# Optimization experiments

Measured on AMD Instinct MI355X. Metric: run time of the kernel, lower is better.

Reference implementation:

```python
import jax, jax.numpy as jnp
import numpy as np

EPS = 1e-6
D_MODEL, D_HEAD, COND_F = 1024, 64, 768
N_HEADS = D_MODEL // D_HEAD
BATCH, SEQ = 2, 2048


def _rope_freqs(d_head, n_heads):
    # RoPE.__init__: dim = d_head // 2; count = n_heads * dim // 4 = n_heads * d_head // 8
    d8 = d_head // 8
    log_min, log_max = np.log(np.pi), np.log(10.0 * np.pi)
    f = np.exp(np.linspace(log_min, log_max, n_heads * d8 + 1, dtype=np.float64)[:-1])
    return jnp.asarray(f.reshape(d8, n_heads).T, dtype=jnp.float32)  # [nh, d8]


def _apply_rotary(x, theta):
    # x: [n, nh, l, e], theta: [n, nh, l, d8]; rotate first 2*d8 channels
    d = theta.shape[-1]
    x1, x2, rest = x[..., :d], x[..., d:2 * d], x[..., 2 * d:]
    cos, sin = jnp.cos(theta), jnp.sin(theta)
    y1 = x1 * cos - x2 * sin
    y2 = x2 * cos + x1 * sin
    return jnp.concatenate([y1, y2, rest], axis=-1)


def setup_inputs() -> dict:
    key = jax.random.key(0)
    ks = jax.random.split(key, 6)
    x = jax.random.normal(ks[0], (BATCH, SEQ, D_MODEL), dtype=jnp.float32)
    pos = jnp.broadcast_to(jnp.arange(SEQ, dtype=jnp.float32), (BATCH, SEQ))[..., None]
    cond = jax.random.normal(ks[1], (BATCH, COND_F), dtype=jnp.float32)
    w_norm = jax.random.normal(ks[2], (D_MODEL, COND_F), dtype=jnp.float32) * 0.02
    w_qkv = jax.random.normal(ks[3], (3 * D_MODEL, D_MODEL), dtype=jnp.float32) * 0.02
    scale = jnp.full((N_HEADS,), 10.0, dtype=jnp.float32)
    w_out = jax.random.normal(ks[4], (D_MODEL, D_MODEL), dtype=jnp.float32) * 0.02
    return {"x": x, "pos": pos, "cond": cond, "w_norm": w_norm,
            "w_qkv": w_qkv, "scale": scale, "w_out": w_out}


def reference(x, pos, cond, w_norm, w_qkv, scale, w_out):
    n, l, d = x.shape
    nh, e = N_HEADS, D_HEAD
    skip = x
    # AdaRMSNorm: scale = (linear(cond) + 1) * rsqrt(mean(x^2))
    cond_scale = cond @ w_norm.T + 1.0                      # [n, d]
    mean_sq = jnp.mean(x * x, axis=-1, keepdims=True)       # [n, l, 1]
    xn = x * (cond_scale[:, None, :] * jax.lax.rsqrt(mean_sq + EPS))
    # QKV projection
    qkv = (xn @ w_qkv.T).reshape(n, l, 3, nh, e)
    q = jnp.transpose(qkv[:, :, 0], (0, 2, 1, 3))           # [n, nh, l, e]
    k = jnp.transpose(qkv[:, :, 1], (0, 2, 1, 3))
    v = jnp.transpose(qkv[:, :, 2], (0, 2, 1, 3))
    # cosine-sim scaling
    sqrt_scale = jnp.sqrt(scale)[None, :, None, None]       # [1, nh, 1, 1]
    q = q * (sqrt_scale * jax.lax.rsqrt(jnp.sum(q * q, axis=-1, keepdims=True) + EPS))
    k = k * (sqrt_scale * jax.lax.rsqrt(jnp.sum(k * k, axis=-1, keepdims=True) + EPS))
    # RoPE: theta = pos[..., None] * freqs -> [n, l, nh, d8] -> [n, nh, l, d8]
    freqs = _rope_freqs(e, nh)
    theta = jnp.transpose(pos[..., None] * freqs, (0, 2, 1, 3))
    q = _apply_rotary(q, theta)
    k = _apply_rotary(k, theta)
    # attention with softmax scale = 1.0
    scores = jnp.einsum('nhle,nhme->nhlm', q, k)
    attn = jax.nn.softmax(scores, axis=-1)
    out = jnp.einsum('nhlm,nhme->nhle', attn, v)
    out = jnp.transpose(out, (0, 2, 1, 3)).reshape(n, l, d)
    return out @ w_out.T + skip
```

## Files before the change

### kernel.cpp

```cpp
#include <hip/hip_runtime.h>
#include <math.h>

#define D_MODEL 1024
#define D_HEAD  64
#define N_HEADS 16
#define COND_F  768
#define BATCH   2
#define SEQ     2048
#define NTOK    (BATCH*SEQ)
#define QKV_N   (3*D_MODEL)

typedef unsigned short u16;
typedef __attribute__((ext_vector_type(4))) float  f32x4;
typedef __attribute__((ext_vector_type(8))) __bf16 bfrag;
typedef __attribute__((ext_vector_type(4))) unsigned short u16x4;
typedef __attribute__((ext_vector_type(8))) unsigned short u16x8;

__device__ __forceinline__ u16 f2bf(float f) {
    unsigned u = __builtin_bit_cast(unsigned, f);
    return (u16)((u + 0x7fffu + ((u >> 16) & 1u)) >> 16);
}
__device__ __forceinline__ float bf2f(u16 h) {
    unsigned u = ((unsigned)h) << 16;
    return __builtin_bit_cast(float, u);
}

__device__ __forceinline__ float fexp2(float x) {
    float y;
    asm("v_exp_f32 %0, %1" : "=v"(y) : "v"(x));
    return y;
}

__device__ __forceinline__ void async16(const void* g, void* l) {
    __builtin_amdgcn_global_load_lds(
        (const __attribute__((address_space(1))) unsigned int*)g,
        (__attribute__((address_space(3))) unsigned int*)l, 16, 0, 0);
}

__global__ __launch_bounds__(256) void prep_kernel(const float* __restrict__ wqkv,
                                                   const float* __restrict__ wout,
                                                   u16* __restrict__ wqkv_b,
                                                   u16* __restrict__ wout_b,
                                                   const float* __restrict__ cond,
                                                   const float* __restrict__ w_norm,
                                                   float* __restrict__ cs,
                                                   const float* __restrict__ pos,
                                                   float2* __restrict__ tab) {
    if (blockIdx.x < 2048) {
        int i = blockIdx.x * 256 + threadIdx.x;
        const int n1 = QKV_N * D_MODEL / 8;
        const float* src; u16* dst; int off;
        if (i < n1) { src = wqkv; dst = wqkv_b; off = i * 8; }
        else        { src = wout; dst = wout_b; off = (i - n1) * 8; }
        float4 a = *(const float4*)(src + off);
        float4 b = *(const float4*)(src + off + 4);
        *(u16x4*)(dst + off)     = (u16x4){f2bf(a.x), f2bf(a.y), f2bf(a.z), f2bf(a.w)};
        *(u16x4*)(dst + off + 4) = (u16x4){f2bf(b.x), f2bf(b.y), f2bf(b.z), f2bf(b.w)};
    } else if (blockIdx.x < 2560) {
        int lane = threadIdx.x & 63, w = threadIdx.x >> 6;
        int wid = (blockIdx.x - 2048) * 4 + w;
        int b = wid >> 10, d = wid & 1023;
        const float* c = cond + b * COND_F;
        const float* wn = w_norm + (size_t)d * COND_F;
        float acc = 0.f;
        #pragma unroll
        for (int kk = 0; kk < 3; ++kk) {
            int j = kk * 256 + lane * 4;
            float4 cv = *(const float4*)(c + j);
            float4 wv = *(const float4*)(wn + j);
            acc += cv.x * wv.x + cv.y * wv.y + cv.z * wv.z + cv.w * wv.w;
        }
        for (int m = 1; m < 64; m <<= 1) acc += __shfl_xor(acc, m);
        if (lane == 0) cs[wid] = acc + 1.0f;
    } else {
        int i = (blockIdx.x - 2560) * 256 + threadIdx.x;
        int j = i & 7, h = (i >> 3) & 15;
        int s = (i >> 7) & 2047, b = i >> 18;
        double lf = 1.1447298858494001741 + (double)(j * 16 + h) * (2.302585092994045684 / 128.0);
        float fr = (float)exp(lf);
        float th = pos[b * SEQ + s] * fr;
        tab[i] = make_float2(cosf(th), sinf(th));
    }
}

__global__ __launch_bounds__(256) void rmsnorm_kernel(const float* __restrict__ x,
                                                      const float* __restrict__ cs,
                                                      u16* __restrict__ xn) {
    int tok = blockIdx.x, t = threadIdx.x;
    int b = tok >> 11;
    const float* xr = x + (size_t)tok * D_MODEL;
    float4 v = *(const float4*)(xr + t * 4);
    float ss = v.x * v.x + v.y * v.y + v.z * v.z + v.w * v.w;
    for (int m = 1; m < 64; m <<= 1) ss += __shfl_xor(ss, m);
    __shared__ float red[4];
    int w = t >> 6;
    if ((t & 63) == 0) red[w] = ss;
    __syncthreads();
    float tot = red[0] + red[1] + red[2] + red[3];
    float r = rsqrtf(tot * (1.0f / D_MODEL) + 1e-6f);
    float4 cv = *(const float4*)(cs + b * D_MODEL + t * 4);
    *(u16x4*)(xn + (size_t)tok * D_MODEL + t * 4) =
        (u16x4){f2bf(v.x * cv.x * r), f2bf(v.y * cv.y * r),
                f2bf(v.z * cv.z * r), f2bf(v.w * cv.w * r)};
}

template<int NT, int MODE>
__global__ __launch_bounds__(256) void gemm_bt(const u16* __restrict__ A, const u16* __restrict__ B,
                                               u16* __restrict__ Cq, u16* __restrict__ Ck,
                                               u16* __restrict__ Cv, float* __restrict__ Cf,
                                               const float* __restrict__ skip,
                                               const float* __restrict__ scale,
                                               const float2* __restrict__ tab,
                                               int M, int N, int K) {
    __shared__ u16 As0[128 * 32];
    __shared__ u16 As1[128 * 32];
    __shared__ u16 Bs0[NT * 32];
    __shared__ u16 Bs1[NT * 32];
    constexpr int FN = NT / 32;
    int tid = threadIdx.x;
    int lane = tid & 63, w = tid >> 6;
    int wr = w >> 1;
    int wc = w & 1;
    int m0 = blockIdx.x * 128, n0 = blockIdx.y * NT;
    f32x4 acc[4][FN] = {};
    const u16* Ag = A + (size_t)m0 * K;
    const u16* Bg = B + (size_t)n0 * K;
    int lr = lane & 15, lq = lane >> 4;

    #define GSTAGE(kt, Ad, Bd) do { \
        _Pragma("unroll") \
        for (int i = 0; i < 2; ++i) { \
            int c = i * 256 + tid; int row = c >> 2, col = c & 3; \
            async16(Ag + (size_t)row * K + (kt) + col * 8, Ad + c * 8); \
        } \
        _Pragma("unroll") \
        for (int i = 0; i < NT / 64; ++i) { \
            int c = i * 256 + tid; int row = c >> 2, col = c & 3; \
            async16(Bg + (size_t)row * K + (kt) + col * 8, Bd + c * 8); \
        } } while (0)

    auto compute = [&](const u16* Asb, const u16* Bsb) {
        bfrag af[4], bfv[FN];
        #pragma unroll
        for (int fm = 0; fm < 4; ++fm)
            af[fm] = *(const bfrag*)&Asb[(wr * 64 + fm * 16 + lr) * 32 + lq * 8];
        #pragma unroll
        for (int fn = 0; fn < FN; ++fn)
            bfv[fn] = *(const bfrag*)&Bsb[(wc * (NT / 2) + fn * 16 + lr) * 32 + lq * 8];
        #pragma unroll
        for (int fm = 0; fm < 4; ++fm)
            #pragma unroll
            for (int fn = 0; fn < FN; ++fn)
                acc[fm][fn] = __builtin_amdgcn_mfma_f32_16x16x32_bf16(af[fm], bfv[fn], acc[fm][fn], 0, 0, 0);
    };

    const int NK = K / 32;
    GSTAGE(0, As0, Bs0);
    __syncthreads();

    for (int t = 0; t < NK; t += 2) {
        if (t + 1 < NK) GSTAGE((t + 1) * 32, As1, Bs1);
        compute(As0, Bs0);
        __syncthreads();
        if (t + 2 < NK) GSTAGE((t + 2) * 32, As0, Bs0);
        if (t + 1 < NK) {
            compute(As1, Bs1);
            __syncthreads();
        }
    }
    #undef GSTAGE

    if (MODE == 1) {
        #pragma unroll
        for (int fm = 0; fm < 4; ++fm)
            #pragma unroll
            for (int fn = 0; fn < FN; ++fn) {
                int rowbase = m0 + wr * 64 + fm * 16 + lq * 4;
                int colbase = n0 + wc * (NT / 2) + fn * 16;
                #pragma unroll
                for (int r = 0; r < 4; ++r) {
                    int row = rowbase + r, col = colbase + lr;
                    Cf[(size_t)row * N + col] = acc[fm][fn][r] + skip[(size_t)row * N + col];
                }
            }
    } else {
        int colbase0 = n0 + wc * 64;
        int sel = colbase0 >> 10;
        int h = (colbase0 >> 6) & 15;
        int bb = m0 >> 11;
        if (sel == 2) {
            #pragma unroll
            for (int fm = 0; fm < 4; ++fm) {
                int sP = (m0 & 2047) + wr * 64 + (fm >> 1) * 32 + 8 * lq + 4 * (fm & 1);
                #pragma unroll
                for (int fn = 0; fn < 4; ++fn) {
                    int e = fn * 16 + lr;
                    u16x4 pk = {f2bf(acc[fm][fn][0]), f2bf(acc[fm][fn][1]),
                                f2bf(acc[fm][fn][2]), f2bf(acc[fm][fn][3])};
                    *(u16x4*)&Cv[((size_t)(bb * N_HEADS + h) * D_HEAD + e) * SEQ + sP] = pk;
                }
            }
        } else {
            u16* p = sel ? Ck : Cq;
            float sq = sqrtf(scale[h]);
            float mult = (sel == 0) ? sq * 1.4426950408889634f : sq;
            #pragma unroll
            for (int fm = 0; fm < 4; ++fm) {
                int s0 = (m0 & 2047) + wr * 64 + fm * 16 + lq * 4;
                #pragma unroll
                for (int r = 0; r < 4; ++r) {
                    float v0 = acc[fm][0][r], v1 = acc[fm][1][r],
                          v2 = acc[fm][2][r], v3 = acc[fm][3][r];
                    float ss = v0 * v0 + v1 * v1 + v2 * v2 + v3 * v3;
                    ss += __shfl_xor(ss, 1); ss += __shfl_xor(ss, 2);
                    ss += __shfl_xor(ss, 4); ss += __shfl_xor(ss, 8);
                    float rs = mult * rsqrtf(ss + 1e-6f);
                    v0 *= rs; v1 *= rs; v2 *= rs; v3 *= rs;
                    float part = __shfl_xor(v0, 8);
                    float2 cs2 = tab[(((size_t)bb * SEQ + (s0 + r)) * 16 + h) * 8 + (lr & 7)];
                    v0 = (lr < 8) ? v0 * cs2.x - part * cs2.y
                                  : v0 * cs2.x + part * cs2.y;
                    size_t rp = ((size_t)(bb * N_HEADS + h) * SEQ + (s0 + r)) * D_HEAD;
                    p[rp + lr]      = f2bf(v0);
                    p[rp + 16 + lr] = f2bf(v1);
                    p[rp + 32 + lr] = f2bf(v2);
                    p[rp + 48 + lr] = f2bf(v3);
                }
            }
        }
    }
}

__global__ __launch_bounds__(512) void attn_kernel(const u16* __restrict__ q,
                                                   const u16* __restrict__ k,
                                                   const u16* __restrict__ vt,
                                                   u16* __restrict__ o_part,
                                                   float* __restrict__ lsum_part) {
    __shared__ u16 Ks0[64 * 64];
    __shared__ u16 Ks1[64 * 64];
    __shared__ u16 Vs0[64 * 64];
    __shared__ u16 Vs1[64 * 64];
    int tid = threadIdx.x, lane = tid & 63, w = tid >> 6;
    int bh = blockIdx.y;
    int qs = blockIdx.x * 256;
    int z = blockIdx.z, nz = gridDim.z;
    int chunk = SEQ / nz;
    int kv0 = z * chunk;
    int lr = lane & 15, lq = lane >> 4;

    bfrag qf[2][2];
    #pragma unroll
    for (int mf = 0; mf < 2; ++mf) {
        const u16* qb = q + ((size_t)bh * SEQ + qs + w * 32 + mf * 16 + lr) * D_HEAD + lq * 8;
        qf[mf][0] = *(const bfrag*)qb;
        qf[mf][1] = *(const bfrag*)(qb + 32);
    }
    bfrag ones;
    #pragma unroll
    for (int j = 0; j < 8; ++j) ones[j] = (__bf16)1.0f;

    f32x4 oacc[2][4] = {};
    f32x4 oacc5[2] = {};
    const u16* kbase = k + (size_t)bh * SEQ * D_HEAD;
    const u16* vbase = vt + (size_t)bh * D_HEAD * SEQ;

    int srow = tid >> 3, scol = (tid & 7) ^ ((tid >> 3) & 7);
    const u16* kg = kbase + (size_t)srow * 64 + scol * 8;
    const u16* vg = vbase + (size_t)srow * SEQ + scol * 8;

    #define STAGE(kt, Kd, Vd) do { \
        async16(kg + (size_t)(kt) * 64, Kd + tid * 8); \
        async16(vg + (kt),              Vd + tid * 8); } while (0)

    auto tile_compute = [&](const u16* Kb, const u16* Vb) {
        f32x4 sacc[2][4] = {};
        __builtin_amdgcn_s_setprio(1);
        #pragma unroll
        for (int nb = 0; nb < 4; ++nb) {
            int row = nb * 16 + lr;
            #pragma unroll
            for (int kb = 0; kb < 2; ++kb) {
                bfrag kf = *(const bfrag*)&Kb[row * 64 + (((kb * 4 + lq) ^ (row & 7)) * 8)];
                sacc[0][nb] = __builtin_amdgcn_mfma_f32_16x16x32_bf16(kf, qf[0][kb], sacc[0][nb], 0, 0, 0);
                sacc[1][nb] = __builtin_amdgcn_mfma_f32_16x16x32_bf16(kf, qf[1][kb], sacc[1][nb], 0, 0, 0);
            }
        }
        __builtin_amdgcn_s_setprio(0);

        #pragma unroll
        for (int kb = 0; kb < 2; ++kb) {
            bfrag pf[2];
            #pragma unroll
            for (int mf = 0; mf < 2; ++mf)
                #pragma unroll
                for (int half = 0; half < 2; ++half) {
                    int nb = kb * 2 + half;
                    #pragma unroll
                    for (int r = 0; r < 4; ++r)
                        pf[mf][half * 4 + r] = (__bf16)fexp2(sacc[mf][nb][r]);
                }
            __builtin_amdgcn_s_setprio(1);
            oacc5[0] = __builtin_amdgcn_mfma_f32_16x16x32_bf16(pf[0], ones, oacc5[0], 0, 0, 0);
            oacc5[1] = __builtin_amdgcn_mfma_f32_16x16x32_bf16(pf[1], ones, oacc5[1], 0, 0, 0);
            #pragma unroll
            for (int eb = 0; eb < 4; ++eb) {
                int row = eb * 16 + lr;
                bfrag vf = *(const bfrag*)&Vb[row * 64 + (((kb * 4 + lq) ^ (row & 7)) * 8)];
                oacc[0][eb] = __builtin_amdgcn_mfma_f32_16x16x32_bf16(pf[kb == 0 ? 0 : 0], vf, oacc[0][eb], 0, 0, 0);
                oacc[1][eb] = __builtin_amdgcn_mfma_f32_16x16x32_bf16(pf[1], vf, oacc[1][eb], 0, 0, 0);
            }
            __builtin_amdgcn_s_setprio(0);
        }
    };

    STAGE(kv0, Ks0, Vs0);
    __syncthreads();

    const int NTILE = chunk / 64;
    for (int t = 0; t < NTILE; t += 2) {
        if (t + 1 < NTILE) STAGE(kv0 + (t + 1) * 64, Ks1, Vs1);
        tile_compute(Ks0, Vs0);
        __syncthreads();
        if (t + 2 < NTILE) STAGE(kv0 + (t + 2) * 64, Ks0, Vs0);
        if (t + 1 < NTILE) {
            tile_compute(Ks1, Vs1);
            __syncthreads();
        }
    }
    #undef STAGE

    int b = bh >> 4, h = bh & 15;
    u16* op = o_part + (size_t)z * NTOK * D_MODEL;
    #pragma unroll
    for (int mf = 0; mf < 2; ++mf) {
        #pragma unroll
        for (int r = 0; r < 4; ++r) {
            int qrow = qs + w * 32 + mf * 16 + lq * 4 + r;
            if (lr == 0)
                lsum_part[((size_t)z * BATCH * N_HEADS + bh) * SEQ + qrow] = oacc5[mf][r];
            #pragma unroll
            for (int eb = 0; eb < 4; ++eb) {
                int e = eb * 16 + lr;
                op[((size_t)b * SEQ + qrow) * D_MODEL + h * D_HEAD + e] = f2bf(oacc[mf][eb][r]);
            }
        }
    }
}

__global__ __launch_bounds__(256) void combine_kernel(const u16* __restrict__ o_part,
                                                      const float* __restrict__ lsum_part,
                                                      u16* __restrict__ out, int Z) {
    int i = blockIdx.x * 256 + threadIdx.x;
    int base = i * 8;
    int t = base >> 10, col = base & 1023;
    int b = t >> 11, s = t & 2047, h = col >> 6;
    size_t li = (size_t)(b * N_HEADS + h) * SEQ + s;
    float lsum = 0.f;
    for (int z = 0; z < Z; ++z) lsum += lsum_part[(size_t)z * BATCH * N_HEADS * SEQ + li];
    float inv = 1.0f / lsum;
    float acc[8] = {};
    for (int z = 0; z < Z; ++z) {
        u16x8 a = *(const u16x8*)(o_part + (size_t)z * NTOK * D_MODEL + base);
        #pragma unroll
        for (int j = 0; j < 8; ++j) acc[j] += bf2f(a[j]);
    }
    u16x8 r;
    #pragma unroll
    for (int j = 0; j < 8; ++j) r[j] = f2bf(acc[j] * inv);
    *(u16x8*)(out + base) = r;
}

extern "C" void kernel_launch(void* const* d_in, const int* in_sizes, int n_in,
                              void* d_out, int out_size, void* d_ws, size_t ws_size,
                              hipStream_t stream) {
    const float* x      = (const float*)d_in[0];
    const float* pos    = (const float*)d_in[1];
    const float* cond   = (const float*)d_in[2];
    const float* w_norm = (const float*)d_in[3];
    const float* w_qkv  = (const float*)d_in[4];
    const float* scale  = (const float*)d_in[5];
    const float* w_out  = (const float*)d_in[6];
    float* out = (float*)d_out;

    char* ws = (char*)d_ws;
    u16* xn     = (u16*)ws;
    u16* wqkv_b = (u16*)(ws + (8u  << 20));
    u16* wout_b = (u16*)(ws + (14u << 20));
    float* cs   = (float*)(ws + (16u << 20));
    u16* qb     = (u16*)(ws + (16u << 20) + (1u << 16));
    const size_t HSZ = (size_t)BATCH * N_HEADS * SEQ * D_HEAD;
    u16* kb = qb + HSZ;
    u16* vt = kb + HSZ;
    u16* o_part   = (u16*)(ws + (41u << 20));
    float2* tab   = (float2*)(ws + (41u << 20));
    u16* attn_o = xn;

    size_t need4 = (41ull << 20) + 4 * ((size_t)NTOK * D_MODEL * 2) + 4 * ((size_t)BATCH * N_HEADS * SEQ * 4);
    int Z = (ws_size >= need4) ? 4 : 2;
    float* lsum_p = (float*)(ws + (41u << 20) + (size_t)Z * NTOK * D_MODEL * 2);

    prep_kernel<<<dim3(4608), dim3(256), 0, stream>>>(w_qkv, w_out, wqkv_b, wout_b,
                                                      cond, w_norm, cs, pos, (float2*)tab);
    rmsnorm_kernel<<<dim3(NTOK), dim3(256), 0, stream>>>(x, cs, xn);
    gemm_bt<128, 0><<<dim3(NTOK / 128, QKV_N / 128), dim3(256), 0, stream>>>(
        xn, wqkv_b, qb, kb, vt, (float*)nullptr, (const float*)nullptr,
        scale, (const float2*)tab, NTOK, QKV_N, D_MODEL);
    attn_kernel<<<dim3(SEQ / 256, BATCH * N_HEADS, Z), dim3(512), 0, stream>>>(
        qb, kb, vt, o_part, lsum_p);
    combine_kernel<<<dim3(NTOK * D_MODEL / 8 / 256), dim3(256), 0, stream>>>(o_part, lsum_p, attn_o, Z);
    gemm_bt<64, 1><<<dim3(NTOK / 128, D_MODEL / 64), dim3(256), 0, stream>>>(
        attn_o, wout_b, nullptr, nullptr, nullptr, out, x,
        (const float*)nullptr, (const float2*)nullptr, NTOK, D_MODEL, D_MODEL);
}
```

Before: 128.9 us.

## Simplify GEMM to single-buffered 128x64 tiles with one row strip per wave

Replaces the double-buffered GEMM, which overlapped async loads with MFMA compute, with a single-buffered loop. That loop syncs twice per 32-wide K step and gives each wave a 32x64 output strip. The QKV projection now uses 128x64 tiles instead of 128x128, which doubles the grid and lowers per-block register and LDS use. This may help occupancy but gives up load/compute overlap and cuts operand reuse from shared memory. A no-op index expression in the attention kernel is also cleaned up.

```diff
diff --git a/kernel.cpp b/kernel.cpp
--- a/kernel.cpp
+++ b/kernel.cpp
@@ -104,7 +104,7 @@
                 f2bf(v.z * cv.z * r), f2bf(v.w * cv.w * r)};
 }
 
-template<int NT, int MODE>
+template<int MODE>
 __global__ __launch_bounds__(256) void gemm_bt(const u16* __restrict__ A, const u16* __restrict__ B,
                                                u16* __restrict__ Cq, u16* __restrict__ Ck,
                                                u16* __restrict__ Cv, float* __restrict__ Cf,
@@ -112,86 +112,59 @@
                                                const float* __restrict__ scale,
                                                const float2* __restrict__ tab,
                                                int M, int N, int K) {
-    __shared__ u16 As0[128 * 32];
-    __shared__ u16 As1[128 * 32];
-    __shared__ u16 Bs0[NT * 32];
-    __shared__ u16 Bs1[NT * 32];
-    constexpr int FN = NT / 32;
+    __shared__ u16 As[128 * 32];
+    __shared__ u16 Bs[64 * 32];
     int tid = threadIdx.x;
     int lane = tid & 63, w = tid >> 6;
-    int wr = w >> 1;
-    int wc = w & 1;
-    int m0 = blockIdx.x * 128, n0 = blockIdx.y * NT;
-    f32x4 acc[4][FN] = {};
+    int m0 = blockIdx.x * 128, n0 = blockIdx.y * 64;
+    f32x4 acc[2][4] = {};
     const u16* Ag = A + (size_t)m0 * K;
     const u16* Bg = B + (size_t)n0 * K;
     int lr = lane & 15, lq = lane >> 4;
 
-    #define GSTAGE(kt, Ad, Bd) do { \
-        _Pragma("unroll") \
-        for (int i = 0; i < 2; ++i) { \
-            int c = i * 256 + tid; int row = c >> 2, col = c & 3; \
-            async16(Ag + (size_t)row * K + (kt) + col * 8, Ad + c * 8); \
-        } \
-        _Pragma("unroll") \
-        for (int i = 0; i < NT / 64; ++i) { \
-            int c = i * 256 + tid; int row = c >> 2, col = c & 3; \
-            async16(Bg + (size_t)row * K + (kt) + col * 8, Bd + c * 8); \
-        } } while (0)
-
-    auto compute = [&](const u16* Asb, const u16* Bsb) {
-        bfrag af[4], bfv[FN];
-        #pragma unroll
-        for (int fm = 0; fm < 4; ++fm)
-            af[fm] = *(const bfrag*)&Asb[(wr * 64 + fm * 16 + lr) * 32 + lq * 8];
-        #pragma unroll
-        for (int fn = 0; fn < FN; ++fn)
-            bfv[fn] = *(const bfrag*)&Bsb[(wc * (NT / 2) + fn * 16 + lr) * 32 + lq * 8];
-        #pragma unroll
-        for (int fm = 0; fm < 4; ++fm)
-            #pragma unroll
-            for (int fn = 0; fn < FN; ++fn)
+    int c1 = 256 + tid;
+    for (int kt = 0; kt < K; kt += 32) {
+        __syncthreads();
+        async16(Ag + (size_t)(tid >> 2) * K + kt + (tid & 3) * 8, &As[tid * 8]);
+        async16(Ag + (size_t)(c1 >> 2) * K + kt + (c1 & 3) * 8, &As[c1 * 8]);
+        async16(Bg + (size_t)(tid >> 2) * K + kt + (tid & 3) * 8, &Bs[tid * 8]);
+        __syncthreads();
+        bfrag af[2], bfv[4];
+        #pragma unroll
+        for (int fm = 0; fm < 2; ++fm)
+            af[fm] = *(const bfrag*)&As[(w * 32 + fm * 16 + lr) * 32 + lq * 8];
+        #pragma unroll
+        for (int fn = 0; fn < 4; ++fn)
+            bfv[fn] = *(const bfrag*)&Bs[(fn * 16 + lr) * 32 + lq * 8];
+        #pragma unroll
+        for (int fm = 0; fm < 2; ++fm)
+            #pragma unroll
+            for (int fn = 0; fn < 4; ++fn)
                 acc[fm][fn] = __builtin_amdgcn_mfma_f32_16x16x32_bf16(af[fm], bfv[fn], acc[fm][fn], 0, 0, 0);
-    };
-
-    const int NK = K / 32;
-    GSTAGE(0, As0, Bs0);
-    __syncthreads();
-
-    for (int t = 0; t < NK; t += 2) {
-        if (t + 1 < NK) GSTAGE((t + 1) * 32, As1, Bs1);
-        compute(As0, Bs0);
-        __syncthreads();
-        if (t + 2 < NK) GSTAGE((t + 2) * 32, As0, Bs0);
-        if (t + 1 < NK) {
-            compute(As1, Bs1);
-            __syncthreads();
-        }
-    }
-    #undef GSTAGE
+    }
 
     if (MODE == 1) {
         #pragma unroll
-        for (int fm = 0; fm < 4; ++fm)
-            #pragma unroll
-            for (int fn = 0; fn < FN; ++fn) {
-                int rowbase = m0 + wr * 64 + fm * 16 + lq * 4;
-                int colbase = n0 + wc * (NT / 2) + fn * 16;
+        for (int fm = 0; fm < 2; ++fm) {
+            int rowbase = m0 + w * 32 + fm * 16 + lq * 4;
+            #pragma unroll
+            for (int fn = 0; fn < 4; ++fn) {
+                int col = n0 + fn * 16 + lr;
                 #pragma unroll
                 for (int r = 0; r < 4; ++r) {
-                    int row = rowbase + r, col = colbase + lr;
+                    int row = rowbase + r;
                     Cf[(size_t)row * N + col] = acc[fm][fn][r] + skip[(size_t)row * N + col];
                 }
             }
+        }
     } else {
-        int colbase0 = n0 + wc * 64;
-        int sel = colbase0 >> 10;
-        int h = (colbase0 >> 6) & 15;
+        int sel = n0 >> 10;
+        int h = (n0 >> 6) & 15;
         int bb = m0 >> 11;
         if (sel == 2) {
             #pragma unroll
-            for (int fm = 0; fm < 4; ++fm) {
-                int sP = (m0 & 2047) + wr * 64 + (fm >> 1) * 32 + 8 * lq + 4 * (fm & 1);
+            for (int fm = 0; fm < 2; ++fm) {
+                int sP = (m0 & 2047) + w * 32 + 8 * lq + 4 * fm;
                 #pragma unroll
                 for (int fn = 0; fn < 4; ++fn) {
                     int e = fn * 16 + lr;
@@ -205,8 +178,8 @@
             float sq = sqrtf(scale[h]);
             float mult = (sel == 0) ? sq * 1.4426950408889634f : sq;
             #pragma unroll
-            for (int fm = 0; fm < 4; ++fm) {
-                int s0 = (m0 & 2047) + wr * 64 + fm * 16 + lq * 4;
+            for (int fm = 0; fm < 2; ++fm) {
+                int s0 = (m0 & 2047) + w * 32 + fm * 16 + lq * 4;
                 #pragma unroll
                 for (int r = 0; r < 4; ++r) {
                     float v0 = acc[fm][0][r], v1 = acc[fm][1][r],
@@ -306,7 +279,7 @@
             for (int eb = 0; eb < 4; ++eb) {
                 int row = eb * 16 + lr;
                 bfrag vf = *(const bfrag*)&Vb[row * 64 + (((kb * 4 + lq) ^ (row & 7)) * 8)];
-                oacc[0][eb] = __builtin_amdgcn_mfma_f32_16x16x32_bf16(pf[kb == 0 ? 0 : 0], vf, oacc[0][eb], 0, 0, 0);
+                oacc[0][eb] = __builtin_amdgcn_mfma_f32_16x16x32_bf16(pf[0], vf, oacc[0][eb], 0, 0, 0);
                 oacc[1][eb] = __builtin_amdgcn_mfma_f32_16x16x32_bf16(pf[1], vf, oacc[1][eb], 0, 0, 0);
             }
             __builtin_amdgcn_s_setprio(0);
@@ -402,13 +375,13 @@
     prep_kernel<<<dim3(4608), dim3(256), 0, stream>>>(w_qkv, w_out, wqkv_b, wout_b,
                                                       cond, w_norm, cs, pos, (float2*)tab);
     rmsnorm_kernel<<<dim3(NTOK), dim3(256), 0, stream>>>(x, cs, xn);
-    gemm_bt<128, 0><<<dim3(NTOK / 128, QKV_N / 128), dim3(256), 0, stream>>>(
+    gemm_bt<0><<<dim3(NTOK / 128, QKV_N / 64), dim3(256), 0, stream>>>(
         xn, wqkv_b, qb, kb, vt, (float*)nullptr, (const float*)nullptr,
         scale, (const float2*)tab, NTOK, QKV_N, D_MODEL);
     attn_kernel<<<dim3(SEQ / 256, BATCH * N_HEADS, Z), dim3(512), 0, stream>>>(
         qb, kb, vt, o_part, lsum_p);
     combine_kernel<<<dim3(NTOK * D_MODEL / 8 / 256), dim3(256), 0, stream>>>(o_part, lsum_p, attn_o, Z);
-    gemm_bt<64, 1><<<dim3(NTOK / 128, D_MODEL / 64), dim3(256), 0, stream>>>(
+    gemm_bt<1><<<dim3(NTOK / 128, D_MODEL / 64), dim3(256), 0, stream>>>(
         attn_o, wout_b, nullptr, nullptr, nullptr, out, x,
         (const float*)nullptr, (const float2*)nullptr, NTOK, D_MODEL, D_MODEL);
 }
```

New measurement: 133.9 us. 3.9% more time.
